# Kernel optimization log

Hardware: AMD Instinct MI355X
Metric: run time of the kernel (lower is better)

Reference implementation:

```python
import jax, jax.numpy as jnp
import numpy as np

GRU_H, H1, H2, ODIM = 256, 128, 64, 3
B, T, HOP = 16, 4000, 80
N = T * HOP  # 320000 samples


def setup_inputs() -> dict:
    key = jax.random.key(0)
    ks = jax.random.split(key, 12)
    inp = {
        'gru_output': jax.random.normal(ks[0], (B, T, GRU_H), dtype=jnp.float32),
        'enhanced': jax.random.normal(ks[1], (B, N), dtype=jnp.float32) * 0.3,
        'noisy': None,
        'W1': jax.random.normal(ks[3], (H1, GRU_H), dtype=jnp.float32) * 0.05,
        'b1': jnp.zeros((H1,), dtype=jnp.float32),
        'a1': jnp.asarray(0.25, dtype=jnp.float32),
        'W2': jax.random.normal(ks[4], (H2, H1), dtype=jnp.float32) * 0.08,
        'b2': jnp.zeros((H2,), dtype=jnp.float32),
        'a2': jnp.asarray(0.25, dtype=jnp.float32),
        'W3': jax.random.normal(ks[5], (ODIM, H2), dtype=jnp.float32) * 0.1,
        'b3': jnp.zeros((ODIM,), dtype=jnp.float32),
    }
    inp['noisy'] = inp['enhanced'] + jax.random.normal(ks[2], (B, N), dtype=jnp.float32) * 0.1
    return inp


def _prelu(x, a):
    return jnp.where(x >= 0, x, a * x)


def _interp_linear(x, n_out):
    # torch F.interpolate(mode='linear', align_corners=False): x [B, T] -> [B, n_out]
    t = x.shape[1]
    src = (jnp.arange(n_out, dtype=jnp.float32) + 0.5) * (t / n_out) - 0.5
    src = jnp.clip(src, 0.0, t - 1)
    i0 = jnp.floor(src).astype(jnp.int32)
    i1 = jnp.minimum(i0 + 1, t - 1)
    w = src - i0.astype(jnp.float32)
    return x[:, i0] * (1.0 - w) + x[:, i1] * w


def _compress(audio, ratio, threshold):
    # soft-knee static gain followed by single-pole IIR smoothing (alpha=0.1)
    env = jnp.abs(audio)
    gain_red = jnp.where(env > threshold, threshold + (env - threshold) / ratio, env)
    gain = jnp.clip(gain_red / (env + 1e-8), 0.1, 2.0)
    alpha = 0.1
    g0 = gain[:, 0]

    def step(carry, g):
        s = alpha * g + (1.0 - alpha) * carry
        return s, s

    _, rest = jax.lax.scan(step, g0, gain[:, 1:].T)  # scan over time, carry [B]
    smoothed = jnp.concatenate([g0[:, None], rest.T], axis=1)
    return audio * smoothed


def reference(gru_output, enhanced, noisy, W1, b1, a1, W2, b2, a2, W3, b3):
    # params MLP (dropout = identity in eval)
    h = _prelu(jnp.einsum('bth,oh->bto', gru_output, W1) + b1, a1)
    h = _prelu(jnp.einsum('bth,oh->bto', h, W2) + b2, a2)
    p = jnp.einsum('bth,oh->bto', h, W3) + b3  # [B, T, 3]

    attack = jax.nn.sigmoid(p[..., 0]) * 0.019 + 0.001
    release = jax.nn.sigmoid(p[..., 1]) * 0.19 + 0.01
    ratio = jnp.clip(jax.nn.softplus(p[..., 2]) + 1.0, 1.0, 20.0)

    n = enhanced.shape[1]
    ratio_i = _interp_linear(ratio, n)
    # attack/release are interpolated in the original but unused by _apply_compression
    _ = _interp_linear(attack, n)
    _ = _interp_linear(release, n)

    residual = noisy - enhanced
    comp_enh = _compress(enhanced, ratio_i, 0.3)
    comp_res = _compress(residual, ratio_i * 0.5, 0.1)

    out = comp_enh + 0.1 * comp_res
    out = out / (jnp.max(jnp.abs(out)) + 1e-8) * jnp.max(jnp.abs(enhanced))
    return out
```

## Files before the change

kernel.cpp:

```cpp
#include <hip/hip_runtime.h>
#include <hip/hip_bf16.h>
#include <math.h>

#define GRU_H 256
#define H1D   128
#define H2D   64
#define BB    16
#define TT    4000
#define NN    320000

typedef __attribute__((ext_vector_type(8))) short short8;
typedef __attribute__((ext_vector_type(4))) float f32x4;

static __device__ __forceinline__ unsigned short f2bf(float x) {
    unsigned u = __float_as_uint(x);
    return (unsigned short)((u + 0x7FFFu + ((u >> 16) & 1u)) >> 16);
}
static __device__ __forceinline__ float bf2f(unsigned short h) {
    return __uint_as_float(((unsigned)h) << 16);
}

#define H1CH 4608
#define W2CH 2304
__global__ __launch_bounds__(256) void mlp_kernel(
    const float* __restrict__ gru, const float* __restrict__ W1,
    const float* __restrict__ b1,  const float* __restrict__ a1p,
    const float* __restrict__ W2,  const float* __restrict__ b2,
    const float* __restrict__ a2p, const float* __restrict__ W3,
    const float* __restrict__ b3,  float* __restrict__ ratio_out,
    unsigned* __restrict__ ws_u)
{
    __shared__ unsigned short smem[36864];
    __shared__ float w3f[64];
    unsigned short* As  = smem;
    unsigned short* Bs  = smem + 4608;
    unsigned short* h2s = smem;
    unsigned short* h1s = smem + 9216;
    unsigned short* W2s = smem + 27648;

    const int t    = threadIdx.x;
    const int wave = t >> 6, lane = t & 63;
    const int lr   = lane & 15, q = lane >> 4;
    const int m0   = blockIdx.x * 128;
    const float a1v = a1p[0], a2v = a2p[0];

    if (blockIdx.x == 0 && t < 2) ws_u[t] = 0u;
    if (t < 64) w3f[t] = W3[2 * H2D + t];

    const int wr = wave >> 1;
    const int wc = wave & 1;
    f32x4 acc1[4][4];
    #pragma unroll
    for (int mi = 0; mi < 4; ++mi)
        #pragma unroll
        for (int ni = 0; ni < 4; ++ni) acc1[mi][ni] = (f32x4){0.f, 0.f, 0.f, 0.f};

    for (int kc = 0; kc < 8; ++kc) {
        const int k0 = kc * 32;
        __syncthreads();
        #pragma unroll
        for (int it = 0; it < 4; ++it) {
            const int idx = t + 256 * it;
            const int row = idx >> 3, c4 = idx & 7;
            float4 g = *(const float4*)(gru + (size_t)(m0 + row) * GRU_H + k0 + c4 * 4);
            ushort4 gh = {f2bf(g.x), f2bf(g.y), f2bf(g.z), f2bf(g.w)};
            *(ushort4*)(As + row * 36 + c4 * 4) = gh;
            float4 w = *(const float4*)(W1 + (size_t)row * GRU_H + k0 + c4 * 4);
            ushort4 wh = {f2bf(w.x), f2bf(w.y), f2bf(w.z), f2bf(w.w)};
            *(ushort4*)(Bs + row * 36 + c4 * 4) = wh;
        }
        __syncthreads();
        short8 af[4], bf[4];
        #pragma unroll
        for (int mi = 0; mi < 4; ++mi) {
            const unsigned short* p = As + (wr * 64 + mi * 16 + lr) * 36 + q * 8;
            ushort4 lo = *(const ushort4*)(p), hi = *(const ushort4*)(p + 4);
            af[mi] = (short8){(short)lo.x, (short)lo.y, (short)lo.z, (short)lo.w,
                              (short)hi.x, (short)hi.y, (short)hi.z, (short)hi.w};
        }
        #pragma unroll
        for (int ni = 0; ni < 4; ++ni) {
            const unsigned short* p = Bs + (wc * 64 + ni * 16 + lr) * 36 + q * 8;
            ushort4 lo = *(const ushort4*)(p), hi = *(const ushort4*)(p + 4);
            bf[ni] = (short8){(short)lo.x, (short)lo.y, (short)lo.z, (short)lo.w,
                              (short)hi.x, (short)hi.y, (short)hi.z, (short)hi.w};
        }
        #pragma unroll
        for (int mi = 0; mi < 4; ++mi)
            #pragma unroll
            for (int ni = 0; ni < 4; ++ni)
                acc1[mi][ni] = __builtin_amdgcn_mfma_f32_16x16x32_bf16(
                    af[mi], bf[ni], acc1[mi][ni], 0, 0, 0);
    }

    #pragma unroll
    for (int ni = 0; ni < 4; ++ni) {
        const int col = wc * 64 + ni * 16 + lr;
        const float bv = b1[col];
        unsigned short* dst = h1s + (col >> 5) * H1CH + (col & 31);
        #pragma unroll
        for (int mi = 0; mi < 4; ++mi) {
            const int rbase = wr * 64 + mi * 16 + q * 4;
            #pragma unroll
            for (int r = 0; r < 4; ++r) {
                float x = acc1[mi][ni][r] + bv;
                x = (x >= 0.f) ? x : a1v * x;
                dst[(rbase + r) * 36] = f2bf(x);
            }
        }
    }
    #pragma unroll
    for (int it = 0; it < 8; ++it) {
        const int idx = t + 256 * it;
        const int row = idx >> 5, c4 = idx & 31;
        float4 w = *(const float4*)(W2 + (size_t)row * H1D + c4 * 4);
        ushort4 wh = {f2bf(w.x), f2bf(w.y), f2bf(w.z), f2bf(w.w)};
        *(ushort4*)(W2s + (c4 >> 3) * W2CH + row * 36 + (c4 & 7) * 4) = wh;
    }
    __syncthreads();

    const int wr2 = wave >> 1;
    const int wc2 = wave & 1;
    f32x4 acc2[4][2];
    #pragma unroll
    for (int mi = 0; mi < 4; ++mi)
        #pragma unroll
        for (int ni = 0; ni < 2; ++ni) acc2[mi][ni] = (f32x4){0.f, 0.f, 0.f, 0.f};

    #pragma unroll
    for (int kc = 0; kc < 4; ++kc) {
        short8 af[4], bf[2];
        #pragma unroll
        for (int mi = 0; mi < 4; ++mi) {
            const unsigned short* p = h1s + kc * H1CH + (wr2 * 64 + mi * 16 + lr) * 36 + q * 8;
            ushort4 lo = *(const ushort4*)(p), hi = *(const ushort4*)(p + 4);
            af[mi] = (short8){(short)lo.x, (short)lo.y, (short)lo.z, (short)lo.w,
                              (short)hi.x, (short)hi.y, (short)hi.z, (short)hi.w};
        }
        #pragma unroll
        for (int ni = 0; ni < 2; ++ni) {
            const unsigned short* p = W2s + kc * W2CH + (wc2 * 32 + ni * 16 + lr) * 36 + q * 8;
            ushort4 lo = *(const ushort4*)(p), hi = *(const ushort4*)(p + 4);
            bf[ni] = (short8){(short)lo.x, (short)lo.y, (short)lo.z, (short)lo.w,
                              (short)hi.x, (short)hi.y, (short)hi.z, (short)hi.w};
        }
        #pragma unroll
        for (int mi = 0; mi < 4; ++mi)
            #pragma unroll
            for (int ni = 0; ni < 2; ++ni)
                acc2[mi][ni] = __builtin_amdgcn_mfma_f32_16x16x32_bf16(
                    af[mi], bf[ni], acc2[mi][ni], 0, 0, 0);
    }

    #pragma unroll
    for (int ni = 0; ni < 2; ++ni) {
        const int col = wc2 * 32 + ni * 16 + lr;
        const float bv = b2[col];
        unsigned short* dst = h2s + (col >> 5) * H1CH + (col & 31);
        #pragma unroll
        for (int mi = 0; mi < 4; ++mi) {
            const int rbase = wr2 * 64 + mi * 16 + q * 4;
            #pragma unroll
            for (int r = 0; r < 4; ++r) {
                float x = acc2[mi][ni][r] + bv;
                x = (x >= 0.f) ? x : a2v * x;
                dst[(rbase + r) * 36] = f2bf(x);
            }
        }
    }
    __syncthreads();

    if (t < 128) {
        float p = b3[2];
        #pragma unroll
        for (int k = 0; k < 64; ++k)
            p = fmaf(bf2f(h2s[(k >> 5) * H1CH + t * 36 + (k & 31)]), w3f[k], p);
        float sp = fmaxf(p, 0.f) + log1pf(expf(-fabsf(p)));
        ratio_out[m0 + t] = fminf(sp + 1.0f, 20.0f);
    }
}

#define CH     256
#define SEGCH  5
#define SEGLEN (CH * SEGCH)
#define SPR    (NN / SEGLEN)

__global__ __launch_bounds__(256) void compress_kernel(
    const float* __restrict__ enh_g, const float* __restrict__ noi_g,
    const float* __restrict__ ratio, float* __restrict__ out,
    unsigned* __restrict__ ws_u)
{
    const int lane = threadIdx.x & 63;
    const int wid  = blockIdx.x * 4 + (threadIdx.x >> 6);
    const int row  = wid / SPR;
    const int seg  = wid - row * SPR;
    const int s0   = seg * SEGLEN;

    const float* __restrict__ enh  = enh_g + (size_t)row * NN;
    const float* __restrict__ noi  = noi_g + (size_t)row * NN;
    const float* __restrict__ rrow = ratio + row * TT;
    float* __restrict__ orow       = out   + (size_t)row * NN;

    float d_lane = 1.f;
    if (lane & 1)  d_lane *= 0.65610000f;
    if (lane & 2)  d_lane *= 0.43046721f;
    if (lane & 4)  d_lane *= 0.18530202f;
    if (lane & 8)  d_lane *= 0.034336838f;
    if (lane & 16) d_lane *= 0.0011790185f;
    if (lane & 32) d_lane *= 1.3900845e-06f;

    float s_e = 0.f, s_r = 0.f;
    float amax_c = 0.f, amax_e = 0.f;

    for (int ci = 0; ci < SEGCH + 1; ++ci) {
        const int cb = s0 - CH + ci * CH;
        const int p0 = cb + 4 * lane;
        const int pc = p0 < 0 ? 0 : p0;
        const float4 e4 = *(const float4*)(enh + pc);
        const float4 x4 = *(const float4*)(noi + pc);

        float pe[4], pr[4];
        float ge0 = 0.f, gr0 = 0.f;
        float ae = 0.f, ar = 0.f;
        #pragma unroll
        for (int k = 0; k < 4; ++k) {
            const float e   = (&e4.x)[k];
            const float x   = (&x4.x)[k];
            const float res = x - e;
            const int n  = p0 + k;
            const int nc = n < 0 ? 0 : n;
            float src = fmaf((float)nc + 0.5f, 0.0125f, -0.5f);
            src = fminf(fmaxf(src, 0.f), 3999.f);
            const int   i0 = (int)src;
            const float w  = src - (float)i0;
            const int   i1 = min(i0 + 1, 3999);
            const float r0 = rrow[i0], r1 = rrow[i1];
            const float rr = r0 * (1.f - w) + r1 * w;
            const float rcp_rr = __builtin_amdgcn_rcpf(rr);

            const float env_e = fabsf(e);
            const float gre = (env_e > 0.3f) ? fmaf(env_e - 0.3f, rcp_rr, 0.3f) : env_e;
            const float ge  = fminf(fmaxf(gre * __builtin_amdgcn_rcpf(env_e + 1e-8f), 0.1f), 2.f);
            const float env_r = fabsf(res);
            const float grr = (env_r > 0.1f) ? fmaf(env_r - 0.1f, 2.f * rcp_rr, 0.1f) : env_r;
            const float gr  = fminf(fmaxf(grr * __builtin_amdgcn_rcpf(env_r + 1e-8f), 0.1f), 2.f);

            if (k == 0) { ge0 = ge; gr0 = gr; }
            ae = fmaf(0.9f, ae, 0.1f * ge);
            ar = fmaf(0.9f, ar, 0.1f * gr);
            pe[k] = ae; pr[k] = ar;
        }

        float Be = pe[3], Br = pr[3];
        #pragma unroll
        for (int l = 0; l < 6; ++l) {
            const int dlt = 1 << l;
            const float ml = (l == 0) ? 0.65610000f  :
                             (l == 1) ? 0.43046721f  :
                             (l == 2) ? 0.18530202f  :
                             (l == 3) ? 0.034336838f :
                             (l == 4) ? 0.0011790185f : 1.3900845e-06f;
            const float me  = (lane >= dlt) ? ml : 0.f;
            const float bse = __shfl_up(Be, dlt, 64);
            const float bsr = __shfl_up(Br, dlt, 64);
            Be = fmaf(me, bse, Be);
            Br = fmaf(me, bsr, Br);
        }
        float Ee = __shfl_up(Be, 1, 64); if (lane == 0) Ee = 0.f;
        float Er = __shfl_up(Br, 1, 64); if (lane == 0) Er = 0.f;

        if (cb == 0) { s_e = __shfl(ge0, 0, 64); s_r = __shfl(gr0, 0, 64); }

        const float Se = fmaf(d_lane, s_e, Ee);
        const float Sr = fmaf(d_lane, s_r, Er);

        if (ci > 0) {
            float4 o;
            #pragma unroll
            for (int k = 0; k < 4; ++k) {
                const float ck = (k == 0) ? 0.9f : (k == 1) ? 0.81f
                               : (k == 2) ? 0.729f : 0.6561f;
                const float sek = fmaf(ck, Se, pe[k]);
                const float srk = fmaf(ck, Sr, pr[k]);
                const float e   = (&e4.x)[k];
                const float res = (&x4.x)[k] - e;
                const float c   = fmaf(0.1f * res, srk, e * sek);
                (&o.x)[k] = c;
                amax_c = fmaxf(amax_c, fabsf(c));
                amax_e = fmaxf(amax_e, fabsf(e));
            }
            *(float4*)(orow + p0) = o;
        }

        const float b63e = __shfl(Be, 63, 64);
        const float b63r = __shfl(Br, 63, 64);
        s_e = fmaf(1.9287e-12f, s_e, b63e);
        s_r = fmaf(1.9287e-12f, s_r, b63r);
    }

    #pragma unroll
    for (int off = 32; off > 0; off >>= 1) {
        amax_c = fmaxf(amax_c, __shfl_xor(amax_c, off, 64));
        amax_e = fmaxf(amax_e, __shfl_xor(amax_e, off, 64));
    }
    __shared__ float red[8];
    const int wv = threadIdx.x >> 6, ln = threadIdx.x & 63;
    if (ln == 0) { red[wv] = amax_c; red[4 + wv] = amax_e; }
    __syncthreads();
    if (threadIdx.x == 0) {
        float mc = fmaxf(fmaxf(red[0], red[1]), fmaxf(red[2], red[3]));
        float me = fmaxf(fmaxf(red[4], red[5]), fmaxf(red[6], red[7]));
        atomicMax(ws_u + 0, __float_as_uint(mc));
        atomicMax(ws_u + 1, __float_as_uint(me));
    }
}

__global__ __launch_bounds__(256) void scale_kernel(float4* __restrict__ out4,
                                                    const unsigned* __restrict__ ws_u)
{
    const float mo = __uint_as_float(ws_u[0]);
    const float me = __uint_as_float(ws_u[1]);
    const float scale = me / (mo + 1e-8f);
    const size_t i = (size_t)blockIdx.x * 256 + threadIdx.x;
    float4 v = out4[i];
    v.x *= scale; v.y *= scale; v.z *= scale; v.w *= scale;
    out4[i] = v;
}

extern "C" void kernel_launch(void* const* d_in, const int* in_sizes, int n_in,
                              void* d_out, int out_size, void* d_ws, size_t ws_size,
                              hipStream_t stream) {
    const float* gru = (const float*)d_in[0];
    const float* enh = (const float*)d_in[1];
    const float* noi = (const float*)d_in[2];
    const float* W1  = (const float*)d_in[3];
    const float* b1  = (const float*)d_in[4];
    const float* a1  = (const float*)d_in[5];
    const float* W2  = (const float*)d_in[6];
    const float* b2  = (const float*)d_in[7];
    const float* a2  = (const float*)d_in[8];
    const float* W3  = (const float*)d_in[9];
    const float* b3  = (const float*)d_in[10];
    float* out = (float*)d_out;

    unsigned* ws_u = (unsigned*)d_ws;
    float* ratio   = (float*)((char*)d_ws + 256);

    mlp_kernel<<<(BB * TT) / 128, 256, 0, stream>>>(gru, W1, b1, a1, W2, b2, a2, W3, b3, ratio, ws_u);
    compress_kernel<<<(BB * (NN / SEGLEN)) / 4, 256, 0, stream>>>(enh, noi, ratio, out, ws_u);
    scale_kernel<<<(BB * NN) / 4 / 256, 256, 0, stream>>>((float4*)out, ws_u);
}
```

Before: 189.6 us.

## Fuse output scaling into compress kernel via grid barrier and register-held outputs

Removes the separate scale kernel. Each compress block now keeps its compressed outputs in registers, waits at a software grid barrier built from an atomic counter until every block has published its max, then writes the scaled result once. This avoids a second full read and write of the output buffer and one kernel launch. The change also prefetches the next chunk's enhanced and noisy float4 loads while the current chunk is processed, and fetches interpolated ratio values by wave shuffles from a per-lane preload instead of global gathers. The barrier only works if all 1000 blocks are resident at once, which launch bounds of 4 blocks per CU are meant to ensure; if they are not, the kernel can deadlock, and the higher register use may also cost occupancy.

```diff
diff --git a/kernel.cpp b/kernel.cpp
--- a/kernel.cpp
+++ b/kernel.cpp
@@ -44,7 +44,7 @@
     const int m0   = blockIdx.x * 128;
     const float a1v = a1p[0], a2v = a2p[0];
 
-    if (blockIdx.x == 0 && t < 2) ws_u[t] = 0u;
+    if (blockIdx.x == 0 && t < 3) ws_u[t] = 0u;
     if (t < 64) w3f[t] = W3[2 * H2D + t];
 
     const int wr = wave >> 1;
@@ -184,8 +184,9 @@
 #define SEGCH  5
 #define SEGLEN (CH * SEGCH)
 #define SPR    (NN / SEGLEN)
-
-__global__ __launch_bounds__(256) void compress_kernel(
+#define NBLK   (BB * SPR / 4)
+
+__global__ __launch_bounds__(256, 4) void compress_kernel(
     const float* __restrict__ enh_g, const float* __restrict__ noi_g,
     const float* __restrict__ ratio, float* __restrict__ out,
     unsigned* __restrict__ ws_u)
@@ -201,6 +202,11 @@
     const float* __restrict__ rrow = ratio + row * TT;
     float* __restrict__ orow       = out   + (size_t)row * NN;
 
+    const float bsrc = fmaf((float)(s0 - CH) + 0.5f, 0.0125f, -0.5f);
+    int base = (int)floorf(bsrc);
+    if (base < 0) base = 0;
+    const float rv = rrow[min(base + lane, TT - 1)];
+
     float d_lane = 1.f;
     if (lane & 1)  d_lane *= 0.65610000f;
     if (lane & 2)  d_lane *= 0.43046721f;
@@ -209,23 +215,36 @@
     if (lane & 16) d_lane *= 0.0011790185f;
     if (lane & 32) d_lane *= 1.3900845e-06f;
 
+    {
+    }
+    const int p0w = s0 - CH + 4 * lane;
+    const int pcw = p0w < 0 ? 0 : p0w;
+    float4 e_cur = *(const float4*)(enh + pcw);
+    float4 x_cur = *(const float4*)(noi + pcw);
+
     float s_e = 0.f, s_r = 0.f;
     float amax_c = 0.f, amax_e = 0.f;
-
+    float cbuf[SEGCH][4];
+
+    #pragma unroll
     for (int ci = 0; ci < SEGCH + 1; ++ci) {
+        float4 e_nxt, x_nxt;
+        if (ci < SEGCH) {
+            const int pn = s0 - CH + (ci + 1) * CH + 4 * lane;
+            e_nxt = *(const float4*)(enh + pn);
+            x_nxt = *(const float4*)(noi + pn);
+        }
+
         const int cb = s0 - CH + ci * CH;
         const int p0 = cb + 4 * lane;
-        const int pc = p0 < 0 ? 0 : p0;
-        const float4 e4 = *(const float4*)(enh + pc);
-        const float4 x4 = *(const float4*)(noi + pc);
 
         float pe[4], pr[4];
         float ge0 = 0.f, gr0 = 0.f;
         float ae = 0.f, ar = 0.f;
         #pragma unroll
         for (int k = 0; k < 4; ++k) {
-            const float e   = (&e4.x)[k];
-            const float x   = (&x4.x)[k];
+            const float e   = (&e_cur.x)[k];
+            const float x   = (&x_cur.x)[k];
             const float res = x - e;
             const int n  = p0 + k;
             const int nc = n < 0 ? 0 : n;
@@ -233,8 +252,10 @@
             src = fminf(fmaxf(src, 0.f), 3999.f);
             const int   i0 = (int)src;
             const float w  = src - (float)i0;
-            const int   i1 = min(i0 + 1, 3999);
-            const float r0 = rrow[i0], r1 = rrow[i1];
+            const int   li0 = i0 - base;
+            const int   li1 = min(i0 + 1, 3999) - base;
+            const float r0 = __shfl(rv, li0, 64);
+            const float r1 = __shfl(rv, li1, 64);
             const float rr = r0 * (1.f - w) + r1 * w;
             const float rcp_rr = __builtin_amdgcn_rcpf(rr);
 
@@ -275,27 +296,26 @@
         const float Sr = fmaf(d_lane, s_r, Er);
 
         if (ci > 0) {
-            float4 o;
             #pragma unroll
             for (int k = 0; k < 4; ++k) {
                 const float ck = (k == 0) ? 0.9f : (k == 1) ? 0.81f
                                : (k == 2) ? 0.729f : 0.6561f;
                 const float sek = fmaf(ck, Se, pe[k]);
                 const float srk = fmaf(ck, Sr, pr[k]);
-                const float e   = (&e4.x)[k];
-                const float res = (&x4.x)[k] - e;
+                const float e   = (&e_cur.x)[k];
+                const float res = (&x_cur.x)[k] - e;
                 const float c   = fmaf(0.1f * res, srk, e * sek);
-                (&o.x)[k] = c;
+                cbuf[ci - 1][k] = c;
                 amax_c = fmaxf(amax_c, fabsf(c));
                 amax_e = fmaxf(amax_e, fabsf(e));
             }
-            *(float4*)(orow + p0) = o;
         }
 
         const float b63e = __shfl(Be, 63, 64);
         const float b63r = __shfl(Br, 63, 64);
         s_e = fmaf(1.9287e-12f, s_e, b63e);
         s_r = fmaf(1.9287e-12f, s_r, b63r);
+        e_cur = e_nxt; x_cur = x_nxt;
     }
 
     #pragma unroll
@@ -313,18 +333,27 @@
         atomicMax(ws_u + 0, __float_as_uint(mc));
         atomicMax(ws_u + 1, __float_as_uint(me));
     }
-}
-
-__global__ __launch_bounds__(256) void scale_kernel(float4* __restrict__ out4,
-                                                    const unsigned* __restrict__ ws_u)
-{
-    const float mo = __uint_as_float(ws_u[0]);
-    const float me = __uint_as_float(ws_u[1]);
+
+    __threadfence();
+    if (threadIdx.x == 0) {
+        __hip_atomic_fetch_add(ws_u + 2, 1u, __ATOMIC_ACQ_REL, __HIP_MEMORY_SCOPE_AGENT);
+        while (__hip_atomic_load(ws_u + 2, __ATOMIC_ACQUIRE, __HIP_MEMORY_SCOPE_AGENT) < NBLK)
+            __builtin_amdgcn_s_sleep(8);
+    }
+    __syncthreads();
+
+    const float mo = __uint_as_float(
+        __hip_atomic_load(ws_u + 0, __ATOMIC_ACQUIRE, __HIP_MEMORY_SCOPE_AGENT));
+    const float me = __uint_as_float(
+        __hip_atomic_load(ws_u + 1, __ATOMIC_ACQUIRE, __HIP_MEMORY_SCOPE_AGENT));
     const float scale = me / (mo + 1e-8f);
-    const size_t i = (size_t)blockIdx.x * 256 + threadIdx.x;
-    float4 v = out4[i];
-    v.x *= scale; v.y *= scale; v.z *= scale; v.w *= scale;
-    out4[i] = v;
+    #pragma unroll
+    for (int ci = 0; ci < SEGCH; ++ci) {
+        float4 o;
+        #pragma unroll
+        for (int k = 0; k < 4; ++k) (&o.x)[k] = cbuf[ci][k] * scale;
+        *(float4*)(orow + s0 + ci * CH + 4 * lane) = o;
+    }
 }
 
 extern "C" void kernel_launch(void* const* d_in, const int* in_sizes, int n_in,
@@ -347,6 +376,5 @@
     float* ratio   = (float*)((char*)d_ws + 256);
 
     mlp_kernel<<<(BB * TT) / 128, 256, 0, stream>>>(gru, W1, b1, a1, W2, b2, a2, W3, b3, ratio, ws_u);
-    compress_kernel<<<(BB * (NN / SEGLEN)) / 4, 256, 0, stream>>>(enh, noi, ratio, out, ws_u);
-    scale_kernel<<<(BB * NN) / 4 / 256, 256, 0, stream>>>((float4*)out, ws_u);
-}
+    compress_kernel<<<NBLK, 256, 0, stream>>>(enh, noi, ratio, out, ws_u);
+}
```

Result: slower. 350.9 us (+85.1%).
